# Performance work log

Measured on AMD Instinct MI355X. Metric: run time of the kernel, lower is better.

The kernel has to match this reference:

```python
import jax, jax.numpy as jnp
import numpy as np

DIM = 256
DIM_HEAD = 32
HEADS = DIM // DIM_HEAD
NUM_TYPES = 2
WS = 7
AGENTS = 6
SCALE = DIM_HEAD ** -0.5


def _rel_pos_index():
    # Static relative-position index for a WS x WS window (torch meshgrid default = 'ij')
    coords = np.stack(np.meshgrid(np.arange(WS), np.arange(WS), indexing='ij'))  # (2,WS,WS)
    cf = coords.reshape(2, -1)                     # (2, WS*WS)
    rel = cf[:, :, None] - cf[:, None, :]          # (2, 49, 49)
    rel = rel.transpose(1, 2, 0).copy()
    rel[:, :, 0] += WS - 1
    rel[:, :, 1] += WS - 1
    rel[:, :, 0] *= 2 * WS - 1
    return jnp.asarray(rel.sum(-1))                # (49, 49) int


def setup_inputs() -> dict:
    key = jax.random.key(0)
    ks = jax.random.split(key, 16)
    B, L, X, Y = 4, AGENTS, 8, 8
    x = jax.random.normal(ks[0], (B, L, X, Y, WS, WS, DIM), dtype=jnp.float32)
    mode = jax.random.randint(ks[1], (B, L), 0, NUM_TYPES)
    s = 0.02
    Wq = jax.random.normal(ks[2], (NUM_TYPES, DIM, DIM), dtype=jnp.float32) * s
    bq = jax.random.normal(ks[3], (NUM_TYPES, DIM), dtype=jnp.float32) * s
    Wk = jax.random.normal(ks[4], (NUM_TYPES, DIM, DIM), dtype=jnp.float32) * s
    bk = jax.random.normal(ks[5], (NUM_TYPES, DIM), dtype=jnp.float32) * s
    Wv = jax.random.normal(ks[6], (NUM_TYPES, DIM, DIM), dtype=jnp.float32) * s
    bv = jax.random.normal(ks[7], (NUM_TYPES, DIM), dtype=jnp.float32) * s
    Wa = jax.random.normal(ks[8], (NUM_TYPES, DIM, DIM), dtype=jnp.float32) * s
    ba = jax.random.normal(ks[9], (NUM_TYPES, DIM), dtype=jnp.float32) * s
    # xavier_uniform over (num_relations, heads, dh, dh): fan based on last two dims
    lim = float(np.sqrt(6.0 / (DIM_HEAD + DIM_HEAD)))
    relation_att = jax.random.uniform(ks[10], (NUM_TYPES * NUM_TYPES, HEADS, DIM_HEAD, DIM_HEAD), minval=-lim, maxval=lim, dtype=jnp.float32)
    relation_msg = jax.random.uniform(ks[11], (NUM_TYPES * NUM_TYPES, HEADS, DIM_HEAD, DIM_HEAD), minval=-lim, maxval=lim, dtype=jnp.float32)
    pos_table = jax.random.normal(ks[12], ((2 * WS - 1) * (2 * WS - 1), HEADS), dtype=jnp.float32)
    return dict(x=x, mode=mode, Wq=Wq, bq=bq, Wk=Wk, bk=bk, Wv=Wv, bv=bv, Wa=Wa, ba=ba,
                relation_att=relation_att, relation_msg=relation_msg, pos_table=pos_table)


def reference(x, mode, Wq, bq, Wk, bk, Wv, bv, Wa, ba, relation_att, relation_msg, pos_table):
    B, L, X, Y, w1, w2, D = x.shape
    h, dh = HEADS, DIM_HEAD
    W = w1 * w2

    def proj(Wt, bt):
        # type-routed Linear: gather per-(b,l) weight, y = x @ W[t].T + b[t]
        y = jnp.einsum('blxyuvd,bled->blxyuve', x, Wt[mode]) + bt[mode][:, :, None, None, None, None, :]
        # b l x y u v (h d) -> b x y h l u v d
        return y.reshape(B, L, X, Y, w1, w2, h, dh).transpose(0, 2, 3, 6, 1, 4, 5, 7)

    q = proj(Wq, bq)[:, :, :, :, :1] * SCALE   # ego agent only (a=1)
    k = proj(Wk, bk)
    v = proj(Wv, bv)

    # relation index for (ego type, agent z type): r[b,z] = mode[b,0]*T + mode[b,z]
    rel_idx = mode[:, :1] * NUM_TYPES + mode           # (B, L)
    w_att = relation_att[rel_idx]                      # (B, L, h, dh, dh)
    w_msg = relation_msg[rel_idx]

    # sim_{pq} = q_p W_att[p,q] k_q
    kw = jnp.einsum('bzhpq,bxyhzefq->bxyhzefp', w_att, k)
    sim = jnp.einsum('bxyhacdp,bxyhzefp->bxyhacdzef', q, kw)  # (B,X,Y,h,1,w1,w2,L,w1,w2)

    # relative position bias, broadcast over agents z
    bias = pos_table[_rel_pos_index()].transpose(2, 0, 1)     # (h, 49, 49)
    sim = sim.reshape(B, X, Y, h, 1, W, L, W) + bias[None, None, None, :, None, :, None, :]

    # softmax over all keys (z, e, f) jointly
    attn = jax.nn.softmax(sim.reshape(B, X, Y, h, W, L * W), axis=-1)
    attn = attn.reshape(B, X, Y, h, 1, w1, w2, L, w1, w2)

    # message: v'_q = sum_p v_p W_msg[p,q]
    v_msg = jnp.einsum('bzhpq,bxyhzefp->bxyhzefq', w_msg, v)
    out = jnp.einsum('bxyhacdzef,bxyhzefq->bxyhacdq', attn, v_msg)

    # b x y h a c d q -> b a x y c d (h q)
    out = out.transpose(0, 4, 1, 2, 5, 6, 3, 7).reshape(B, 1, X, Y, w1, w2, D)

    # type-routed output projection for ego agent
    m0 = mode[:, :1]
    out = jnp.einsum('blxyuvd,bled->blxyuve', out, Wa[m0]) + ba[m0][:, :, None, None, None, None, :]
    return out
```

## Files before the change

### kernel.cpp

```cpp
#include <hip/hip_runtime.h>

typedef unsigned short u16;
typedef unsigned int   u32;
typedef _Float16 f16;
typedef _Float16 h2  __attribute__((ext_vector_type(2)));
typedef _Float16 h8  __attribute__((ext_vector_type(8)));
typedef float    fx4 __attribute__((ext_vector_type(4)));

#define SCALE_Q 0.17677669529663687f

__device__ __forceinline__ u16 f2h_bits(float f){
  union{ f16 h; u16 u; } v; v.h = (f16)f; return v.u;
}
__device__ __forceinline__ u32 packh2(float a, float b){
  union{ h2 h; u32 u; } v; v.h = h2{(f16)a, (f16)b}; return v.u;
}
__device__ __forceinline__ h2 as_h2(u32 x){
  union{ u32 u; h2 h; } v; v.u = x; return v.h;
}
__device__ __forceinline__ h8 as_h8(uint4 u){
  union{ uint4 u; h8 h; } v; v.u = u; return v.h;
}

__global__ void flag_fill(float* out, int n, float v){
  int i = blockIdx.x*256 + threadIdx.x;
  if (i < n) out[i] = v;
}

__global__ __launch_bounds__(512) void fuse_all(
    const float* __restrict__ Wk, const float* __restrict__ Wv,
    const float* __restrict__ Ratt, const float* __restrict__ Rmsg,
    const float* __restrict__ Wq, const float* __restrict__ Wa,
    const float* __restrict__ bk, const float* __restrict__ bv,
    u16* __restrict__ Wft, float* __restrict__ bff,
    u16* __restrict__ Wqf, u16* __restrict__ Waf)
{
  const int blk = blockIdx.x;
  const int n = threadIdx.x;
  if (blk < 1024){
    const int rel = blk >> 8, d = blk & 255, ml = rel & 1;
    float acc = 0.f;
    if (n < 256) {
      const int h = n >> 5, p = n & 31;
      const float* wcol = Wk + (size_t)ml*65536 + (size_t)(h*32)*256 + d;
      const float* rrow = Ratt + ((size_t)(rel*8 + h)*32 + p)*32;
      #pragma unroll
      for (int q = 0; q < 32; ++q) acc += wcol[q*256] * rrow[q];
    } else {
      const int n2 = n - 256, h = n2 >> 5, qq = n2 & 31;
      const float* wcol = Wv + (size_t)ml*65536 + (size_t)(h*32)*256 + d;
      const float* rcol = Rmsg + ((size_t)(rel*8 + h)*32)*32 + qq;
      #pragma unroll
      for (int p2 = 0; p2 < 32; ++p2) acc += wcol[p2*256] * rcol[p2*32];
    }
    Wft[(size_t)rel*131072 + (size_t)(d >> 5)*16384 + (size_t)n*32 + (d & 31)] = f2h_bits(acc);
  } else if (blk < 1028){
    const int rel = blk - 1024, ml = rel & 1;
    float acc = 0.f;
    if (n < 256) {
      const int h = n >> 5, p = n & 31;
      const float* rrow = Ratt + ((size_t)(rel*8 + h)*32 + p)*32;
      #pragma unroll
      for (int q = 0; q < 32; ++q) acc += bk[ml*256 + h*32 + q] * rrow[q];
    } else {
      const int n2 = n - 256, h = n2 >> 5, qq = n2 & 31;
      const float* rcol = Rmsg + ((size_t)(rel*8 + h)*32)*32 + qq;
      #pragma unroll
      for (int p2 = 0; p2 < 32; ++p2) acc += bv[ml*256 + h*32 + p2] * rcol[p2*32];
    }
    bff[rel*512 + n] = acc;
  } else {
    const int bb = blk - 1028;
    const int t = bb >> 8, d = bb & 255;
    if (n < 256){
      float v = Wq[(size_t)t*65536 + (size_t)n*256 + d] * SCALE_Q;
      Wqf[(size_t)t*65536 + (size_t)(d >> 5)*8192 + (size_t)n*32 + (d & 31)] = f2h_bits(v);
    } else {
      const int e = n - 256;
      float v = Wa[(size_t)t*65536 + (size_t)e*256 + d];
      Waf[(size_t)t*65536 + (size_t)(d >> 5)*8192 + (size_t)e*32 + (d & 31)] = f2h_bits(v);
    }
  }
}

#define ASTRIDE 264

__global__ __launch_bounds__(512) void gemm_kwv(
    const float* __restrict__ x, const int* __restrict__ mode,
    const u16* __restrict__ Wft, const float* __restrict__ bff,
    u16* __restrict__ kw, u16* __restrict__ vm, int b0)
{
  __shared__ u16 Smem[64*ASTRIDE];
  const int rowT  = blockIdx.x;
  const int bloc = rowT / 294;
  const int rem  = rowT % 294;
  const int l = rem / 49, tile = rem % 49;
  const int b = b0 + bloc;
  const int rel = mode[b*6]*2 + mode[b*6 + l];
  const float* Abase = x + ((size_t)(b*6 + l)*3136 + (size_t)tile*64)*256;
  const int tid  = threadIdx.x;
  const int wave = tid >> 6, lane = tid & 63;
  const int quad = lane >> 4, l15 = lane & 15;

  const u16* Bp = Wft + (size_t)rel*131072 + (size_t)((wave << 6) + l15)*32 + (quad << 3);

  uint4 breg[3][4];
  #pragma unroll
  for (int s = 0; s < 3; ++s)
    #pragma unroll
    for (int j = 0; j < 4; ++j){
      const u16* ap = Bp + (size_t)s*16384 + j*512;
      asm volatile("global_load_dwordx4 %0, %1, off" : "=v"(breg[s][j]) : "v"(ap));
    }

  #pragma unroll
  for (int i = 0; i < 8; ++i){
    float4 f = *(const float4*)(Abase + (size_t)i*2048 + tid*4);
    const int row = i*8 + (tid >> 6), col = (tid & 63)*4;
    uint2 pk; pk.x = packh2(f.x, f.y); pk.y = packh2(f.z, f.w);
    *(uint2*)&Smem[row*ASTRIDE + col] = pk;
  }
  __syncthreads();

  fx4 acc[4][4];
  #pragma unroll
  for (int mt = 0; mt < 4; ++mt)
    #pragma unroll
    for (int j = 0; j < 4; ++j) acc[mt][j] = fx4{0,0,0,0};

  const u16* As = &Smem[l15*ASTRIDE + (quad << 3)];

  #pragma unroll
  for (int s = 0; s < 8; ++s){
    if (s >= 3 && s <= 5)      { asm volatile("s_waitcnt vmcnt(8)" ::: "memory"); }
    else if (s == 6)           { asm volatile("s_waitcnt vmcnt(4)" ::: "memory"); }
    else if (s == 7)           { asm volatile("s_waitcnt vmcnt(0)" ::: "memory"); }
    __builtin_amdgcn_sched_barrier(0);
    h8 af[4];
    #pragma unroll
    for (int mt = 0; mt < 4; ++mt)
      af[mt] = *(const h8*)(As + (mt*16)*ASTRIDE + s*32);
    const int slot = s % 3;
    #pragma unroll
    for (int j = 0; j < 4; ++j){
      h8 bf = as_h8(breg[slot][j]);
      #pragma unroll
      for (int mt = 0; mt < 4; ++mt)
        acc[mt][j] = __builtin_amdgcn_mfma_f32_16x16x32_f16(af[mt], bf, acc[mt][j], 0, 0, 0);
    }
    if (s < 5){
      #pragma unroll
      for (int j = 0; j < 4; ++j){
        const u16* ap = Bp + (size_t)(s + 3)*16384 + j*512;
        asm volatile("global_load_dwordx4 %0, %1, off" : "=v"(breg[slot][j]) : "v"(ap));
      }
    }
  }

  const int row_ = tid >> 3;
  const int hsel = tid & 7;
  const int r_g  = tile*64 + row_;
  const int xy   = r_g / 49, ef = r_g - xy*49;

  #pragma unroll
  for (int half = 0; half < 2; ++half){
    __syncthreads();
    if ((wave >> 2) == half){
      #pragma unroll
      for (int j = 0; j < 4; ++j){
        const int n   = wave*64 + j*16 + l15;
        const int col = n & 255;
        const float bias = bff[rel*512 + n];
        #pragma unroll
        for (int mt = 0; mt < 4; ++mt){
          #pragma unroll
          for (int reg = 0; reg < 4; ++reg){
            const int row = mt*16 + quad*4 + reg;
            Smem[row*ASTRIDE + col] = f2h_bits(acc[mt][j][reg] + bias);
          }
        }
      }
    }
    __syncthreads();
    u16* dbuf = half ? vm : kw;
    u16* dst  = dbuf + ((((size_t)(bloc*64 + xy)*8 + hsel)*6 + l)*49 + ef)*32;
    const u16* srcl = &Smem[row_*ASTRIDE + hsel*32];
    *(uint4*)(dst)      = *(const uint4*)(srcl);
    *(uint4*)(dst + 8)  = *(const uint4*)(srcl + 8);
    *(uint4*)(dst + 16) = *(const uint4*)(srcl + 16);
    *(uint4*)(dst + 24) = *(const uint4*)(srcl + 24);
  }
}

__global__ __launch_bounds__(256, 2) void gemm_qp(
    const float* __restrict__ x, const int* __restrict__ mode,
    const u16* __restrict__ Wqf, const float* __restrict__ bq,
    u16* __restrict__ qbuf)
{
  __shared__ u16 Smem[32*ASTRIDE];
  const int rowT = blockIdx.x;
  const int b = rowT / 98, tile = rowT % 98;
  const int m0 = mode[b*6];
  const float* Abase = x + ((size_t)(b*6)*3136 + (size_t)tile*32)*256;
  const int tid = threadIdx.x;
  const int wave = tid >> 6, lane = tid & 63;
  const int quad = lane >> 4, l15 = lane & 15;

  const u16* Bp = Wqf + (size_t)m0*65536 + (size_t)((wave << 6) + l15)*32 + (quad << 3);
  uint4 breg[32];
  #pragma unroll
  for (int s = 0; s < 8; ++s)
    #pragma unroll
    for (int j = 0; j < 4; ++j){
      const u16* ap = Bp + (size_t)s*8192 + j*512;
      asm volatile("global_load_dwordx4 %0, %1, off" : "=v"(breg[s*4+j]) : "v"(ap));
    }

  {
    const int r = tid >> 3, cseg = (tid & 7)*32;
    const float* src = Abase + (size_t)r*256 + cseg;
    u16* dst = &Smem[r*ASTRIDE + cseg];
    #pragma unroll
    for (int i = 0; i < 4; ++i){
      float4 f0 = *(const float4*)(src + i*8);
      float4 f1 = *(const float4*)(src + i*8 + 4);
      uint4 pk;
      pk.x = packh2(f0.x, f0.y); pk.y = packh2(f0.z, f0.w);
      pk.z = packh2(f1.x, f1.y); pk.w = packh2(f1.z, f1.w);
      *(uint4*)(dst + i*8) = pk;
    }
  }
  __syncthreads();

  fx4 acc[2][4];
  #pragma unroll
  for (int mt = 0; mt < 2; ++mt)
    #pragma unroll
    for (int j = 0; j < 4; ++j) acc[mt][j] = fx4{0,0,0,0};

  const u16* As0 = &Smem[l15*ASTRIDE + (quad << 3)];
  const u16* As1 = As0 + 16*ASTRIDE;
  asm volatile("s_waitcnt vmcnt(0)" ::: "memory");
  __builtin_amdgcn_sched_barrier(0);
  #pragma unroll
  for (int s = 0; s < 8; ++s){
    h8 af0 = *(const h8*)(As0 + s*32);
    h8 af1 = *(const h8*)(As1 + s*32);
    #pragma unroll
    for (int j = 0; j < 4; ++j){
      h8 bf = as_h8(breg[s*4+j]);
      acc[0][j] = __builtin_amdgcn_mfma_f32_16x16x32_f16(af0, bf, acc[0][j], 0, 0, 0);
      acc[1][j] = __builtin_amdgcn_mfma_f32_16x16x32_f16(af1, bf, acc[1][j], 0, 0, 0);
    }
  }

  __syncthreads();
  #pragma unroll
  for (int j = 0; j < 4; ++j){
    const int n = wave*64 + j*16 + l15;
    const float bias = bq[m0*256 + n] * SCALE_Q;
    #pragma unroll
    for (int mt = 0; mt < 2; ++mt)
      #pragma unroll
      for (int reg = 0; reg < 4; ++reg){
        const int row = mt*16 + quad*4 + reg;
        Smem[row*ASTRIDE + n] = f2h_bits(acc[mt][j][reg] + bias);
      }
  }
  __syncthreads();
  {
    const int row_ = tid >> 3, hsel = tid & 7;
    const int r_g = tile*32 + row_;
    const int xy = r_g / 49, ef = r_g - xy*49;
    u16* dst = qbuf + (((size_t)(b*64 + xy)*8 + hsel)*49 + ef)*32;
    const u16* srcl = &Smem[row_*ASTRIDE + hsel*32];
    *(uint4*)(dst)      = *(const uint4*)(srcl);
    *(uint4*)(dst + 8)  = *(const uint4*)(srcl + 8);
    *(uint4*)(dst + 16) = *(const uint4*)(srcl + 16);
    *(uint4*)(dst + 24) = *(const uint4*)(srcl + 24);
  }
}

__global__ __launch_bounds__(64) void attn_kernel(
    const u16* __restrict__ qbuf, const u16* __restrict__ kw,
    const u16* __restrict__ vm,   const float* __restrict__ post,
    u16* __restrict__ aout, int b0)
{
  __shared__ u32 Ks[64*16];
  __shared__ u16 VT[32*64];
  __shared__ u16 PQ[64*64];
  __shared__ float poss[169];

  const int bloc  = blockIdx.x >> 9;
  const int local = blockIdx.x & 511;
  const int h = local & 7, xy = local >> 3;
  const int bxy = (b0 + bloc)*64 + xy;
  const int lane = threadIdx.x;
  const int quad = lane >> 4, l15 = lane & 15;

  for (int i = lane; i < 169; i += 64) poss[i] = post[i*8 + h];
  for (int i = lane; i < 240; i += 64) Ks[784 + i] = 0;
  for (int i = lane; i < 512; i += 64){
    const int p = i >> 4, ke = 48 + (i & 15);
    VT[p*64 + ((((ke >> 3) ^ (p & 7)) & 7) << 3) + (ke & 7)] = 0;
  }
  { const u16* qsrc = qbuf + (size_t)(bxy*8 + h)*1568;
    for (int i = lane; i < 196; i += 64)
      *(uint4*)&PQ[(i >> 2)*32 + (i & 3)*8] = *(const uint4*)(qsrc + (size_t)i*8);
    const uint4 z4 = make_uint4(0,0,0,0);
    for (int i = lane; i < 60; i += 64)
      *(uint4*)&PQ[1568 + i*8] = z4;
  }
  __syncthreads();

  h8 qf[4];
  #pragma unroll
  for (int nt = 0; nt < 4; ++nt)
    qf[nt] = *(const h8*)&PQ[(nt*16 + l15)*32 + quad*8];

  fx4 bias[4][4];
  { int qa[4], qb[4];
    #pragma unroll
    for (int nt = 0; nt < 4; ++nt){
      const int qi = nt*16 + l15; qa[nt] = qi/7; qb[nt] = qi - qa[nt]*7;
    }
    #pragma unroll
    for (int mt = 0; mt < 4; ++mt)
      #pragma unroll
      for (int reg = 0; reg < 4; ++reg){
        const int ke = mt*16 + quad*4 + reg;
        const int ka = ke/7, kb = ke - ka*7;
        #pragma unroll
        for (int nt = 0; nt < 4; ++nt){
          const int qi = nt*16 + l15;
          float bv;
          if (ke > 48)      bv = -1e30f;
          else if (qi > 48) bv = 0.f;
          else              bv = poss[(qa[nt] - ka + 6)*13 + (qb[nt] - kb + 6)];
          bias[mt][nt][reg] = bv;
        }
      }
  }

  const size_t kvbase = ((size_t)(bloc*64 + xy)*8 + h)*6;
  float mprev[4], lsum[4];
  fx4 Oacc[2][4];
  #pragma unroll
  for (int nt = 0; nt < 4; ++nt){
    mprev[nt] = -1e30f; lsum[nt] = 0.f;
    Oacc[0][nt] = fx4{0,0,0,0}; Oacc[1][nt] = fx4{0,0,0,0};
  }

  for (int z = 0; z < 6; ++z){
    __syncthreads();
    { const uint4* ksrc = (const uint4*)((const u32*)kw + (kvbase + z)*784);
      for (int i = lane; i < 196; i += 64) ((uint4*)Ks)[i] = ksrc[i];
      const uint4* vsrc = (const uint4*)((const u32*)vm + (kvbase + z)*784);
      for (int i = lane; i < 196; i += 64){
        uint4 v4 = vsrc[i];
        const int ef = i >> 2, pb = (i & 3)*8;
        const int c0 = ef >> 3;
        u16* vt = VT + (ef & 7);
        vt[(pb+0)*64 + ((c0 ^ 0) << 3)] = (u16)(v4.x & 0xFFFFu);
        vt[(pb+1)*64 + ((c0 ^ 1) << 3)] = (u16)(v4.x >> 16);
        vt[(pb+2)*64 + ((c0 ^ 2) << 3)] = (u16)(v4.y & 0xFFFFu);
        vt[(pb+3)*64 + ((c0 ^ 3) << 3)] = (u16)(v4.y >> 16);
        vt[(pb+4)*64 + ((c0 ^ 4) << 3)] = (u16)(v4.z & 0xFFFFu);
        vt[(pb+5)*64 + ((c0 ^ 5) << 3)] = (u16)(v4.z >> 16);
        vt[(pb+6)*64 + ((c0 ^ 6) << 3)] = (u16)(v4.w & 0xFFFFu);
        vt[(pb+7)*64 + ((c0 ^ 7) << 3)] = (u16)(v4.w >> 16);
      } }
    __syncthreads();

    h8 kf[4];
    #pragma unroll
    for (int mt = 0; mt < 4; ++mt)
      kf[mt] = *(const h8*)((const u16*)Ks + (mt*16 + l15)*32 + quad*8);
    fx4 S[4][4];
    #pragma unroll
    for (int mt = 0; mt < 4; ++mt)
      #pragma unroll
      for (int nt = 0; nt < 4; ++nt)
        S[mt][nt] = __builtin_amdgcn_mfma_f32_16x16x32_f16(kf[mt], qf[nt], bias[mt][nt], 0, 0, 0);

    #pragma unroll
    for (int nt = 0; nt < 4; ++nt){
      float cm = S[0][nt][0];
      #pragma unroll
      for (int mt = 0; mt < 4; ++mt)
        #pragma unroll
        for (int r = 0; r < 4; ++r) cm = fmaxf(cm, S[mt][nt][r]);
      cm = fmaxf(cm, __shfl_xor(cm, 16));
      cm = fmaxf(cm, __shfl_xor(cm, 32));
      const float mnew = fmaxf(mprev[nt], cm);
      const float alpha = __expf(mprev[nt] - mnew);
      mprev[nt] = mnew;
      float sum = 0.f;
      #pragma unroll
      for (int mt = 0; mt < 4; ++mt)
        #pragma unroll
        for (int r = 0; r < 4; ++r){
          float e = __expf(S[mt][nt][r] - mnew); S[mt][nt][r] = e; sum += e;
        }
      sum += __shfl_xor(sum, 16);
      sum += __shfl_xor(sum, 32);
      lsum[nt] = lsum[nt]*alpha + sum;
      #pragma unroll
      for (int r = 0; r < 4; ++r){ Oacc[0][nt][r] *= alpha; Oacc[1][nt][r] *= alpha; }
    }

    #pragma unroll
    for (int nt = 0; nt < 4; ++nt){
      const int qi = nt*16 + l15;
      u16* prow = &PQ[qi*64 + ((quad & 1) << 2)];
      #pragma unroll
      for (int mt = 0; mt < 4; ++mt){
        const int chk = (mt*2 + (quad >> 1)) ^ (l15 & 7);
        uint2 w;
        w.x = packh2(S[mt][nt][0], S[mt][nt][1]);
        w.y = packh2(S[mt][nt][2], S[mt][nt][3]);
        *(uint2*)(prow + (chk << 3)) = w;
      }
    }
    __syncthreads();

    #pragma unroll
    for (int ks = 0; ks < 2; ++ks){
      h8 vf[2];
      #pragma unroll
      for (int m2 = 0; m2 < 2; ++m2)
        vf[m2] = *(const h8*)&VT[(m2*16 + l15)*64 + (((ks*4 + quad) ^ (l15 & 7)) << 3)];
      #pragma unroll
      for (int nt = 0; nt < 4; ++nt){
        h8 pf = *(const h8*)&PQ[(nt*16 + l15)*64 + (((ks*4 + quad) ^ (l15 & 7)) << 3)];
        Oacc[0][nt] = __builtin_amdgcn_mfma_f32_16x16x32_f16(vf[0], pf, Oacc[0][nt], 0, 0, 0);
        Oacc[1][nt] = __builtin_amdgcn_mfma_f32_16x16x32_f16(vf[1], pf, Oacc[1][nt], 0, 0, 0);
      }
    }
  }

  __syncthreads();
  #pragma unroll
  for (int nt = 0; nt < 4; ++nt){
    const int qi = nt*16 + l15;
    if (qi < 49){
      const float inv = 1.f / lsum[nt];
      #pragma unroll
      for (int m2 = 0; m2 < 2; ++m2){
        uint2 w;
        w.x = packh2(Oacc[m2][nt][0]*inv, Oacc[m2][nt][1]*inv);
        w.y = packh2(Oacc[m2][nt][2]*inv, Oacc[m2][nt][3]*inv);
        *(uint2*)&PQ[qi*32 + m2*16 + quad*4] = w;
      }
    }
  }
  __syncthreads();
  { u16* obase = aout + (size_t)bxy*12544 + h*32;
    for (int i = lane; i < 196; i += 64){
      const int r = i >> 2, c = (i & 3)*8;
      *(uint4*)(obase + (size_t)r*256 + c) = *(const uint4*)&PQ[r*32 + c];
    }
  }
}

__global__ __launch_bounds__(256, 2) void gemm_op(
    const u16* __restrict__ aout, const int* __restrict__ mode,
    const u16* __restrict__ Waf, const float* __restrict__ ba,
    float* __restrict__ outp)
{
  __shared__ float Smf[32*260];
  u16* Smem = (u16*)Smf;
  const int rowT = blockIdx.x;
  const int b = rowT / 98, tile = rowT % 98;
  const int m0 = mode[b*6];
  const u16* Abase = aout + ((size_t)b*3136 + (size_t)tile*32)*256;
  const int tid = threadIdx.x;
  const int wave = tid >> 6, lane = tid & 63;
  const int quad = lane >> 4, l15 = lane & 15;

  const u16* Bp = Waf + (size_t)m0*65536 + (size_t)((wave << 6) + l15)*32 + (quad << 3);
  uint4 breg[32];
  #pragma unroll
  for (int s = 0; s < 8; ++s)
    #pragma unroll
    for (int j = 0; j < 4; ++j){
      const u16* ap = Bp + (size_t)s*8192 + j*512;
      asm volatile("global_load_dwordx4 %0, %1, off" : "=v"(breg[s*4+j]) : "v"(ap));
    }

  {
    const int r = tid >> 3, cseg = (tid & 7)*32;
    const u16* src = Abase + (size_t)r*256 + cseg;
    u16* dst = &Smem[r*ASTRIDE + cseg];
    #pragma unroll
    for (int i = 0; i < 4; ++i)
      *(uint4*)(dst + i*8) = *(const uint4*)(src + i*8);
  }
  __syncthreads();

  fx4 acc[2][4];
  #pragma unroll
  for (int mt = 0; mt < 2; ++mt)
    #pragma unroll
    for (int j = 0; j < 4; ++j) acc[mt][j] = fx4{0,0,0,0};

  const u16* As0 = &Smem[l15*ASTRIDE + (quad << 3)];
  const u16* As1 = As0 + 16*ASTRIDE;
  asm volatile("s_waitcnt vmcnt(0)" ::: "memory");
  __builtin_amdgcn_sched_barrier(0);
  #pragma unroll
  for (int s = 0; s < 8; ++s){
    h8 af0 = *(const h8*)(As0 + s*32);
    h8 af1 = *(const h8*)(As1 + s*32);
    #pragma unroll
    for (int j = 0; j < 4; ++j){
      h8 bf = as_h8(breg[s*4+j]);
      acc[0][j] = __builtin_amdgcn_mfma_f32_16x16x32_f16(af0, bf, acc[0][j], 0, 0, 0);
      acc[1][j] = __builtin_amdgcn_mfma_f32_16x16x32_f16(af1, bf, acc[1][j], 0, 0, 0);
    }
  }

  __syncthreads();
  #pragma unroll
  for (int j = 0; j < 4; ++j){
    const int n = wave*64 + j*16 + l15;
    const float bias = ba[m0*256 + n];
    #pragma unroll
    for (int mt = 0; mt < 2; ++mt)
      #pragma unroll
      for (int reg = 0; reg < 4; ++reg){
        const int row = mt*16 + quad*4 + reg;
        Smf[row*260 + n] = acc[mt][j][reg] + bias;
      }
  }
  __syncthreads();
  {
    const int row_ = tid >> 3, seg = (tid & 7)*32;
    const int rowg = b*3136 + tile*32 + row_;
    float* dst = outp + (size_t)rowg*256 + seg;
    const float* srcl = &Smf[row_*260 + seg];
    #pragma unroll
    for (int i = 0; i < 8; ++i)
      *(float4*)(dst + i*4) = *(const float4*)(srcl + i*4);
  }
}

extern "C" void kernel_launch(void* const* d_in, const int* in_sizes, int n_in,
                              void* d_out, int out_size, void* d_ws, size_t ws_size,
                              hipStream_t stream)
{
  float* outp = (float*)d_out;
  const int FLAG_GRID = (out_size + 255)/256;

  if (n_in != 13) { flag_fill<<<FLAG_GRID,256,0,stream>>>(outp, out_size, 2000.f); return; }
  if (in_sizes[0] != 4*6*64*49*256) { flag_fill<<<FLAG_GRID,256,0,stream>>>(outp, out_size, 3000.f); return; }
  if (in_sizes[1] != 24) { flag_fill<<<FLAG_GRID,256,0,stream>>>(outp, out_size, 4000.f); return; }

  const size_t SZ_WFT  = (size_t)4*512*256*2;
  const size_t SZ_BFF  = (size_t)4*512*sizeof(float);
  const size_t SZ_WQF  = (size_t)2*256*256*2;
  const size_t SZ_WAF  = (size_t)2*256*256*2;
  const size_t SZ_Q    = (size_t)12544*256*2;
  const size_t SZ_AOUT = (size_t)12544*256*2;
  const size_t SZ_KW1  = (size_t)64*8*6*49*32*2;
  const size_t SZ_VM1  = SZ_KW1;
  const size_t FIXED   = SZ_WFT + SZ_BFF + SZ_WQF + SZ_WAF + SZ_Q + SZ_AOUT;
  if (ws_size < FIXED + SZ_KW1 + SZ_VM1) { flag_fill<<<FLAG_GRID,256,0,stream>>>(outp, out_size, 1000.f); return; }

  int nb = 1;
  if (ws_size >= FIXED + 4*(SZ_KW1 + SZ_VM1)) nb = 4;
  else if (ws_size >= FIXED + 2*(SZ_KW1 + SZ_VM1)) nb = 2;

  const float* x    = (const float*)d_in[0];
  const int*   mode = (const int*)d_in[1];
  const float* Wq   = (const float*)d_in[2];
  const float* bq   = (const float*)d_in[3];
  const float* Wk   = (const float*)d_in[4];
  const float* bk   = (const float*)d_in[5];
  const float* Wv   = (const float*)d_in[6];
  const float* bv   = (const float*)d_in[7];
  const float* Wa   = (const float*)d_in[8];
  const float* ba   = (const float*)d_in[9];
  const float* Ratt = (const float*)d_in[10];
  const float* Rmsg = (const float*)d_in[11];
  const float* post = (const float*)d_in[12];

  char* w = (char*)d_ws;
  u16* Wft   = (u16*)w;   w += SZ_WFT;
  float* bff = (float*)w; w += SZ_BFF;
  u16* Wqf   = (u16*)w;   w += SZ_WQF;
  u16* Waf   = (u16*)w;   w += SZ_WAF;
  u16* qbuf  = (u16*)w;   w += SZ_Q;
  u16* aout  = (u16*)w;   w += SZ_AOUT;
  u16* kwbuf = (u16*)w;   w += (size_t)nb*SZ_KW1;
  u16* vmbuf = (u16*)w;   w += (size_t)nb*SZ_VM1;

  fuse_all<<<1540, 512, 0, stream>>>(Wk, Wv, Ratt, Rmsg, Wq, Wa, bk, bv,
                                     Wft, bff, Wqf, Waf);
  gemm_qp<<<392, 256, 0, stream>>>(x, mode, Wqf, bq, qbuf);
  for (int b0 = 0; b0 < 4; b0 += nb) {
    gemm_kwv<<<nb*294, 512, 0, stream>>>(x, mode, Wft, bff, kwbuf, vmbuf, b0);
    attn_kernel<<<nb*512, 64, 0, stream>>>(qbuf, kwbuf, vmbuf, post, aout, b0);
  }
  gemm_op<<<392, 256, 0, stream>>>(aout, mode, Waf, ba, outp);
}
```

Baseline: 271.4 us.

## Double-buffer K/V tiles in attention kernel and replace barriers with lgkmcnt waits

Double-buffers the per-agent K and V tiles in shared memory. The next agent's K/V is loaded into registers from global memory while the current agent's MFMAs run, then written into the alternate buffer. Because the block is a single 64-thread wavefront, the __syncthreads barriers are replaced with s_waitcnt lgkmcnt(0) plus a scheduling barrier. This hides global load latency and removes the barrier cost, but doubles K/V shared memory and adds register pressure for the prefetched data.

```diff
diff --git a/kernel.cpp b/kernel.cpp
--- a/kernel.cpp
+++ b/kernel.cpp
@@ -281,13 +281,29 @@
   }
 }
 
+#define LGKM0  do{ asm volatile("s_waitcnt lgkmcnt(0)" ::: "memory"); \
+                   __builtin_amdgcn_sched_barrier(0); }while(0)
+
+__device__ __forceinline__ void scatter_v(u16* VTb, int i4, uint4 vv){
+  const int ef = i4 >> 2, pb = (i4 & 3)*8, c0 = ef >> 3;
+  u16* vt = VTb + (ef & 7);
+  vt[(pb+0)*64 + ((c0 ^ 0) << 3)] = (u16)(vv.x & 0xFFFFu);
+  vt[(pb+1)*64 + ((c0 ^ 1) << 3)] = (u16)(vv.x >> 16);
+  vt[(pb+2)*64 + ((c0 ^ 2) << 3)] = (u16)(vv.y & 0xFFFFu);
+  vt[(pb+3)*64 + ((c0 ^ 3) << 3)] = (u16)(vv.y >> 16);
+  vt[(pb+4)*64 + ((c0 ^ 4) << 3)] = (u16)(vv.z & 0xFFFFu);
+  vt[(pb+5)*64 + ((c0 ^ 5) << 3)] = (u16)(vv.z >> 16);
+  vt[(pb+6)*64 + ((c0 ^ 6) << 3)] = (u16)(vv.w & 0xFFFFu);
+  vt[(pb+7)*64 + ((c0 ^ 7) << 3)] = (u16)(vv.w >> 16);
+}
+
 __global__ __launch_bounds__(64) void attn_kernel(
     const u16* __restrict__ qbuf, const u16* __restrict__ kw,
     const u16* __restrict__ vm,   const float* __restrict__ post,
     u16* __restrict__ aout, int b0)
 {
-  __shared__ u32 Ks[64*16];
-  __shared__ u16 VT[32*64];
+  __shared__ u32 Ks[2*64*16];
+  __shared__ u16 VT[2*32*64];
   __shared__ u16 PQ[64*64];
   __shared__ float poss[169];
 
@@ -298,11 +314,17 @@
   const int lane = threadIdx.x;
   const int quad = lane >> 4, l15 = lane & 15;
 
+  const size_t kvbase = ((size_t)(bloc*64 + xy)*8 + h)*6;
+
   for (int i = lane; i < 169; i += 64) poss[i] = post[i*8 + h];
-  for (int i = lane; i < 240; i += 64) Ks[784 + i] = 0;
-  for (int i = lane; i < 512; i += 64){
-    const int p = i >> 4, ke = 48 + (i & 15);
-    VT[p*64 + ((((ke >> 3) ^ (p & 7)) & 7) << 3) + (ke & 7)] = 0;
+  for (int i = lane; i < 480; i += 64){
+    const int bb = i / 240, o = i - bb*240;
+    Ks[bb*1024 + 784 + o] = 0;
+  }
+  for (int i = lane; i < 1024; i += 64){
+    const int bb = i >> 9, r = i & 511;
+    const int p = r >> 4, ke = 48 + (r & 15);
+    VT[bb*2048 + p*64 + ((((ke >> 3) ^ (p & 7)) & 7) << 3) + (ke & 7)] = 0;
   }
   { const u16* qsrc = qbuf + (size_t)(bxy*8 + h)*1568;
     for (int i = lane; i < 196; i += 64)
@@ -311,7 +333,12 @@
     for (int i = lane; i < 60; i += 64)
       *(uint4*)&PQ[1568 + i*8] = z4;
   }
-  __syncthreads();
+  { const uint4* ksrc = (const uint4*)((const u32*)kw + kvbase*784);
+    for (int i = lane; i < 196; i += 64) ((uint4*)Ks)[i] = ksrc[i];
+    const uint4* vsrc = (const uint4*)((const u32*)vm + kvbase*784);
+    for (int i = lane; i < 196; i += 64) scatter_v(VT, i, vsrc[i]);
+  }
+  LGKM0;
 
   h8 qf[4];
   #pragma unroll
@@ -342,7 +369,6 @@
       }
   }
 
-  const size_t kvbase = ((size_t)(bloc*64 + xy)*8 + h)*6;
   float mprev[4], lsum[4];
   fx4 Oacc[2][4];
   #pragma unroll
@@ -351,31 +377,24 @@
     Oacc[0][nt] = fx4{0,0,0,0}; Oacc[1][nt] = fx4{0,0,0,0};
   }
 
+  int cur = 0;
   for (int z = 0; z < 6; ++z){
-    __syncthreads();
-    { const uint4* ksrc = (const uint4*)((const u32*)kw + (kvbase + z)*784);
-      for (int i = lane; i < 196; i += 64) ((uint4*)Ks)[i] = ksrc[i];
-      const uint4* vsrc = (const uint4*)((const u32*)vm + (kvbase + z)*784);
-      for (int i = lane; i < 196; i += 64){
-        uint4 v4 = vsrc[i];
-        const int ef = i >> 2, pb = (i & 3)*8;
-        const int c0 = ef >> 3;
-        u16* vt = VT + (ef & 7);
-        vt[(pb+0)*64 + ((c0 ^ 0) << 3)] = (u16)(v4.x & 0xFFFFu);
-        vt[(pb+1)*64 + ((c0 ^ 1) << 3)] = (u16)(v4.x >> 16);
-        vt[(pb+2)*64 + ((c0 ^ 2) << 3)] = (u16)(v4.y & 0xFFFFu);
-        vt[(pb+3)*64 + ((c0 ^ 3) << 3)] = (u16)(v4.y >> 16);
-        vt[(pb+4)*64 + ((c0 ^ 4) << 3)] = (u16)(v4.z & 0xFFFFu);
-        vt[(pb+5)*64 + ((c0 ^ 5) << 3)] = (u16)(v4.z >> 16);
-        vt[(pb+6)*64 + ((c0 ^ 6) << 3)] = (u16)(v4.w & 0xFFFFu);
-        vt[(pb+7)*64 + ((c0 ^ 7) << 3)] = (u16)(v4.w >> 16);
-      } }
-    __syncthreads();
+    uint4 kn0, kn1, kn2, kn3, vn0, vn1, vn2, vn3;
+    if (z < 5){
+      const uint4* ksrc = (const uint4*)((const u32*)kw + (kvbase + z + 1)*784);
+      const uint4* vsrc = (const uint4*)((const u32*)vm + (kvbase + z + 1)*784);
+      kn0 = ksrc[lane]; kn1 = ksrc[64 + lane]; kn2 = ksrc[128 + lane];
+      vn0 = vsrc[lane]; vn1 = vsrc[64 + lane]; vn2 = vsrc[128 + lane];
+      if (lane < 4){ kn3 = ksrc[192 + lane]; vn3 = vsrc[192 + lane]; }
+    }
+
+    const u32* KsC = Ks + cur*1024;
+    const u16* VTC = VT + cur*2048;
 
     h8 kf[4];
     #pragma unroll
     for (int mt = 0; mt < 4; ++mt)
-      kf[mt] = *(const h8*)((const u16*)Ks + (mt*16 + l15)*32 + quad*8);
+      kf[mt] = *(const h8*)((const u16*)KsC + (mt*16 + l15)*32 + quad*8);
     fx4 S[4][4];
     #pragma unroll
     for (int mt = 0; mt < 4; ++mt)
@@ -422,14 +441,14 @@
         *(uint2*)(prow + (chk << 3)) = w;
       }
     }
-    __syncthreads();
+    LGKM0;
 
     #pragma unroll
     for (int ks = 0; ks < 2; ++ks){
       h8 vf[2];
       #pragma unroll
       for (int m2 = 0; m2 < 2; ++m2)
-        vf[m2] = *(const h8*)&VT[(m2*16 + l15)*64 + (((ks*4 + quad) ^ (l15 & 7)) << 3)];
+        vf[m2] = *(const h8*)&VTC[(m2*16 + l15)*64 + (((ks*4 + quad) ^ (l15 & 7)) << 3)];
       #pragma unroll
       for (int nt = 0; nt < 4; ++nt){
         h8 pf = *(const h8*)&PQ[(nt*16 + l15)*64 + (((ks*4 + quad) ^ (l15 & 7)) << 3)];
@@ -437,9 +456,25 @@
         Oacc[1][nt] = __builtin_amdgcn_mfma_f32_16x16x32_f16(vf[1], pf, Oacc[1][nt], 0, 0, 0);
       }
     }
-  }
-
-  __syncthreads();
+
+    if (z < 5){
+      u32* KsN = Ks + (cur ^ 1)*1024;
+      u16* VTN = VT + (cur ^ 1)*2048;
+      ((uint4*)KsN)[lane]       = kn0;
+      ((uint4*)KsN)[64 + lane]  = kn1;
+      ((uint4*)KsN)[128 + lane] = kn2;
+      scatter_v(VTN, lane,       vn0);
+      scatter_v(VTN, 64 + lane,  vn1);
+      scatter_v(VTN, 128 + lane, vn2);
+      if (lane < 4){
+        ((uint4*)KsN)[192 + lane] = kn3;
+        scatter_v(VTN, 192 + lane, vn3);
+      }
+    }
+    LGKM0;
+    cur ^= 1;
+  }
+
   #pragma unroll
   for (int nt = 0; nt < 4; ++nt){
     const int qi = nt*16 + l15;
@@ -454,7 +489,7 @@
       }
     }
   }
-  __syncthreads();
+  LGKM0;
   { u16* obase = aout + (size_t)bxy*12544 + h*32;
     for (int i = lane; i < 196; i += 64){
       const int r = i >> 2, c = (i & 3)*8;
```

Measured after the change: 252.9 us. -6.8%, faster.
